# Kernel tuning notes

Measured on AMD Instinct MI355X. Metric: run time of the kernel, lower is better.

Reference implementation:

```python
import jax, jax.numpy as jnp
import numpy as np

N = 4096          # residues (2 chains x 2048)
CHAINS = 2
LMAX = 2
L = (LMAX + 1) ** 2            # 9 spherical coefficients
BBC = 32                       # bb_channels
NBB = 3                        # n_bb_atoms - 1
SPH = BBC + NBB                # 35 sphere channels fed to attention
KNN = 20
LRK = 40
HEADS = 8
HC = 32
VC = HC // 4                   # attn_value_channels = 8
EDGE_F = 32                    # 16 RBF + 16 positional
L_IDX = np.repeat(np.arange(LMAX + 1), 2 * np.arange(LMAX + 1) + 1)  # degree of each of the 9 coeffs


def so3_linear(x, w, b):
    # x: [N,L,Cin]; w: [LMAX+1,Cin,Cout] shared across m within each degree l; bias only on l=0
    out = jnp.einsum('nlc,lcd->nld', x, w[L_IDX])
    return out.at[:, 0, :].add(b)


def _rbf(d):
    mu = jnp.linspace(0.0, 20.0, 16)
    sigma = 20.0 / 16
    return jnp.exp(-(((d[..., None] - mu) / sigma) ** 2))


def _edge_pos_embed(src, dst):
    d = (src - dst).astype(jnp.float32)
    freq = jnp.exp(jnp.arange(0, 16, 2, dtype=jnp.float32) * (-np.log(10000.0) / 16))
    ang = d[:, None] * freq
    return jnp.concatenate([jnp.cos(ang), jnp.sin(ang)], axis=-1)


def setup_inputs():
    key = jax.random.key(0)
    ks = jax.random.split(key, 16)
    n = lambda i, shp, s=1.0: jax.random.normal(ks[i], shp) * s
    return {
        'X_ca': n(0, (N, 3), 10.0),
        'bb_rel': n(1, (N, NBB, 3)),
        'bb_features': n(2, (N, L, BBC)),
        'batch': jnp.repeat(jnp.arange(CHAINS), N // CHAINS),
        'x_mask': jax.random.uniform(ks[3], (N,)) < 0.02,
        'noising_mask': jax.random.uniform(ks[4], (N,)) < 0.5,
        'attn_w1': n(5, (2 * SPH + EDGE_F, HC), 0.05), 'attn_b1': jnp.zeros((HC,)),
        'attn_w2': n(6, (HC, HEADS), 0.05), 'attn_b2': jnp.zeros((HEADS,)),
        'wv': n(7, (LMAX + 1, SPH, HEADS * VC), 0.05), 'bv': jnp.zeros((HEADS * VC,)),
        'wo': n(8, (LMAX + 1, HEADS * VC, BBC), 0.05), 'bo': jnp.zeros((BBC,)),
        'wg': n(9, (BBC, BBC), 0.05), 'bg': jnp.zeros((BBC,)),
        'wf': n(10, (LMAX + 1, BBC, BBC), 0.05), 'bf': jnp.zeros((BBC,)),
        'w_xca': n(11, (LMAX + 1, BBC, 1), 0.05), 'b_xca': jnp.zeros((1,)),
        'w_gate': n(12, (BBC, 1), 0.05), 'b_gate': jnp.zeros((1,)),
        'w_bb': n(13, (LMAX + 1, BBC, NBB), 0.05), 'b_bb': jnp.zeros((NBB,)),
    }


def reference(X_ca, bb_rel, bb_features, batch, x_mask, noising_mask,
              attn_w1, attn_b1, attn_w2, attn_b2, wv, bv, wo, bo, wg, bg, wf, bf,
              w_xca, b_xca, w_gate, b_gate, w_bb, b_bb):
    Nn = X_ca.shape[0]
    BIG = jnp.float32(1e30)
    # ---- graph construction (knn_graph + sample_inv_cubic_edges) ----
    x2 = jnp.sum(X_ca * X_ca, axis=-1)
    D2 = jnp.maximum(x2[:, None] + x2[None, :] - 2.0 * (X_ca @ X_ca.T), 0.0)  # [N,N]
    same = batch[:, None] == batch[None, :]
    eye = jnp.eye(Nn, dtype=bool)
    mask_pair = x_mask[:, None] | x_mask[None, :]
    invalid = (~same) | eye | mask_pair
    knn_idx = jax.lax.top_k(-jnp.where(invalid, BIG, D2), KNN)[1]   # [N,KNN] sources per target
    # long-range: inverse-cubic distance weights, Gumbel top-k sampling, excluding knn picks
    logits = jnp.where(invalid, -BIG, -1.5 * jnp.log(D2 + 1e-6))
    rows = jnp.arange(Nn)[:, None]
    logits = logits.at[rows, knn_idx].set(-BIG)
    gumb = jax.random.gumbel(jax.random.key(1), (Nn, Nn))
    lr_idx = jax.lax.top_k(logits + gumb, LRK)[1]                   # [N,LRK]
    src = jnp.concatenate([knn_idx.reshape(-1), lr_idx.reshape(-1)])
    dst = jnp.concatenate([jnp.repeat(jnp.arange(Nn), KNN), jnp.repeat(jnp.arange(Nn), LRK)])
    # ---- edge features: RBF(dist) + relative positional embedding ----
    dvec = X_ca[src] - X_ca[dst]
    dist = jnp.linalg.norm(dvec, axis=-1)
    edge_feat = jnp.concatenate([_rbf(dist), _edge_pos_embed(src, dst)], axis=-1)  # [M,32]
    # ---- assemble SO3 node embedding [N,L,35] ----
    node = jnp.zeros((Nn, L, SPH), X_ca.dtype)
    node = node.at[:, :, :BBC].set(bb_features)
    node = node.at[:, 1:4, BBC:].set(jnp.swapaxes(bb_rel, -1, -2))  # l=1 coeffs carry bb_rel
    node = node.at[:, 0, SPH - 1].set(noising_mask.astype(X_ca.dtype))
    # ---- equivariant graph attention (simplified TransBlockV2) ----
    inv = node[:, 0, :]                                             # invariant (l=0) features
    a_in = jnp.concatenate([inv[src], inv[dst], edge_feat], axis=-1)
    h = jax.nn.silu(a_in @ attn_w1 + attn_b1)
    logit = h @ attn_w2 + attn_b2                                   # [M,HEADS]
    mx = jax.ops.segment_max(logit, dst, num_segments=Nn)
    p = jnp.exp(logit - mx[dst])
    Z = jax.ops.segment_sum(p, dst, num_segments=Nn)
    alpha = p / (Z[dst] + 1e-9)                                     # segment softmax per target/head
    v = so3_linear(node, wv, bv)[src].reshape(-1, L, HEADS, VC)     # gather source values
    msg = (v * alpha[:, None, :, None]).reshape(-1, L, HEADS * VC)
    agg = jax.ops.segment_sum(msg, dst, num_segments=Nn)            # scatter to targets
    out = so3_linear(agg, wo, bo)                                   # [N,L,32]
    gate = jax.nn.silu(out[:, 0, :] @ wg + bg)                      # invariant-gated FFN
    out = out + so3_linear(out, wf, bf) * gate[:, None, :]
    # ---- coordinate / backbone updates ----
    upd_x = so3_linear(out, w_xca, b_xca)                           # [N,L,1]
    vec = upd_x[:, 1:4, 0]                                          # l=1 -> 3-vector
    g2 = jax.nn.softplus(out[:, 0, :] @ w_gate + b_gate)            # [N,1]
    new_X = X_ca + jnp.where(noising_mask[:, None], vec * g2, 0.0)
    upd_bb = so3_linear(out, w_bb, b_bb)                            # [N,L,3]
    dbb = jnp.swapaxes(upd_bb[:, 1:4, :], -1, -2)                   # [N,3,3]
    new_bb = bb_rel + jnp.where(noising_mask[:, None, None], dbb, 0.0)
    return new_X, new_bb, out
```

## Files before the change

kernel.cpp:

```cpp
#include <hip/hip_runtime.h>
#include <hip/hip_bf16.h>
#include <stdint.h>

#define NN 4096
#define CS 2048
#define KNN 20
#define LRK 40
#define EPN 60
#define NE (NN*EPN)
#define SPHC 35
#define BBCC 32
#define NHEAD 8
#define HVD 64
#define HCD 32
#define LT 9
#define MAXC 384

#define INVAL_D2 0xFFFFFFFEu
#define CONSUMED 0xFFFFFFFFu

__device__ __forceinline__ float fast_exp(float x) {
  return __builtin_amdgcn_exp2f(x * 1.4426950408889634f);
}
__device__ __forceinline__ float fast_cos(float a) {
  float rev = a * 0.15915494309189535f;
  rev = rev - __builtin_rintf(rev);
  return __builtin_amdgcn_cosf(rev);
}
__device__ __forceinline__ float fast_sin(float a) {
  float rev = a * 0.15915494309189535f;
  rev = rev - __builtin_rintf(rev);
  return __builtin_amdgcn_sinf(rev);
}

__device__ __forceinline__ float neglogu_f(int i, int j) {
  uint32_t c = ((uint32_t)(i & 2047) << 12) | (uint32_t)j;
  const uint32_t ks0 = 0u, ks1 = 1u, ks2 = 0x1BD11BDBu;
  uint32_t x0 = c + ks0;
  uint32_t x1 = (c + 0x800000u) + ks1;
#define TF_R(r) { x0 += x1; x1 = (x1 << (r)) | (x1 >> (32 - (r))); x1 ^= x0; }
  TF_R(13) TF_R(15) TF_R(26) TF_R(6)   x0 += ks1; x1 += ks2 + 1u;
  TF_R(17) TF_R(29) TF_R(16) TF_R(24)  x0 += ks2; x1 += ks0 + 2u;
  TF_R(13) TF_R(15) TF_R(26) TF_R(6)   x0 += ks0; x1 += ks1 + 3u;
  TF_R(17) TF_R(29) TF_R(16) TF_R(24)  x0 += ks1; x1 += ks2 + 4u;
  TF_R(13) TF_R(15) TF_R(26) TF_R(6)   x0 += ks2; x1 += ks0 + 5u;
#undef TF_R
  uint32_t b = (i >= 2048) ? x1 : x0;
  float u = __uint_as_float((b >> 9) | 0x3F800000u) - 1.0f;
  u = u + 1.17549435e-38f;
  return -logf(u);
}

__global__ void prep_kernel(const float* __restrict__ X,
                            const int* __restrict__ batch,
                            const int* __restrict__ xmask,
                            float4* __restrict__ Xw, uint32_t* __restrict__ bm) {
#pragma clang fp contract(off)
  int n = blockIdx.x * blockDim.x + threadIdx.x;
  if (n >= NN) return;
  float x = X[n*3+0], y = X[n*3+1], z = X[n*3+2];
  float x2 = (x*x + y*y) + z*z;
  Xw[n] = make_float4(x, y, z, x2);
  bm[n] = ((uint32_t)batch[n] << 1) | (xmask[n] ? 1u : 0u);
}

__global__ __launch_bounds__(256) void nodeproj_kernel(const float* __restrict__ bbf,
                                                       const int* __restrict__ nmask,
                                                       const float* __restrict__ w1,
                                                       const float* __restrict__ b1,
                                                       float* __restrict__ Pn,
                                                       float* __restrict__ Pd) {
  int tid = threadIdx.x;
  int t = tid & 31;
  int n = blockIdx.x * 8 + (tid >> 5);
  float bv_ = bbf[(size_t)n * (LT*BBCC) + t];
  float an = 0.f, ad = b1[t];
  #pragma unroll 8
  for (int c = 0; c < BBCC; c++) {
    float bc = __shfl(bv_, (tid & 32) + c, 64);
    an = fmaf(bc, w1[c * HCD + t], an);
    ad = fmaf(bc, w1[(SPHC + c) * HCD + t], ad);
  }
  float nm = nmask[n] ? 1.f : 0.f;
  an = fmaf(nm, w1[34 * HCD + t], an);
  ad = fmaf(nm, w1[69 * HCD + t], ad);
  Pn[n * HCD + t] = an;
  Pd[n * HCD + t] = ad;
}

__device__ __forceinline__ void sel2l(uint32_t* val, uint32_t* hist2,
                                      uint32_t* candk, uint32_t* candp,
                                      uint32_t* sh, int* sel,
                                      int k, int base, int cb, int tid) {
  {
    uint4* h4 = (uint4*)hist2;
    uint4 z; z.x = 0; z.y = 0; z.z = 0; z.w = 0;
    h4[tid] = z; h4[tid + 256] = z;
  }
  if (tid == 0) { sh[2] = 0; sh[3] = 0; }
  __syncthreads();
  #pragma unroll
  for (int q = 0; q < 8; q++) {
    uint32_t key = val[tid + (q << 8)];
    atomicAdd(&hist2[key >> 21], 1u);
  }
  __syncthreads();
  uint32_t h[8], s = 0;
  #pragma unroll
  for (int q = 0; q < 8; q++) { h[q] = hist2[tid*8 + q]; s += h[q]; }
  uint32_t cum = s;
  #pragma unroll
  for (int off = 1; off < 64; off <<= 1) {
    uint32_t o = __shfl_up(cum, off, 64);
    if ((tid & 63) >= off) cum += o;
  }
  if ((tid & 63) == 63) sh[8 + (tid >> 6)] = cum;
  __syncthreads();
  uint32_t woff = 0;
  for (int w = 0; w < (tid >> 6); w++) woff += sh[8 + w];
  uint32_t cumAll = cum + woff;
  uint32_t cumBefore = cumAll - s;
  uint32_t rk = (uint32_t)k;
  if (rk > cumBefore && rk <= cumAll) {
    uint32_t rloc = rk - cumBefore, lp = 0;
    bool done = false;
    #pragma unroll
    for (int q = 0; q < 8; q++) {
      lp += h[q];
      if (!done && rloc <= lp) { sh[0] = (uint32_t)(tid*8 + q); sh[1] = rloc - (lp - h[q]); done = true; }
    }
  }
  __syncthreads();
  const uint32_t B = sh[0], r = sh[1];
  #pragma unroll
  for (int q = 0; q < 8; q++) {
    int pos = tid + (q << 8);
    uint32_t key = val[pos];
    if ((key >> 21) == B) {
      uint32_t idx = atomicAdd(&sh[2], 1u);
      if (idx < MAXC) { candk[idx] = key; candp[idx] = (uint32_t)pos; }
    }
  }
  __syncthreads();
  int m = (int)sh[2]; if (m > MAXC) m = MAXC;
  if (tid < 64) {
    for (int ci = tid; ci < m; ci += 64) {
      unsigned long long k64 = ((unsigned long long)candk[ci] << 32) | candp[ci];
      uint32_t rank = 0;
      for (int j = 0; j < m; j++) {
        unsigned long long o = ((unsigned long long)candk[j] << 32) | candp[j];
        rank += (o < k64) ? 1u : 0u;
      }
      if (rank == r - 1) { sh[0] = candk[ci]; sh[1] = candp[ci]; }
    }
  }
  __syncthreads();
  const uint32_t vstar = sh[0], istar = sh[1];
  #pragma unroll
  for (int q = 0; q < 8; q++) {
    int pos = tid + (q << 8);
    uint32_t key = val[pos];
    if (key < vstar || (key == vstar && (uint32_t)pos <= istar)) {
      uint32_t slot = atomicAdd(&sh[3], 1u);
      sel[base + (int)slot] = cb + pos;
    }
  }
  __syncthreads();
}

__global__ __launch_bounds__(256) void select_kernel(const float4* __restrict__ Xw,
                                                     const uint32_t* __restrict__ bm,
                                                     int* __restrict__ srcO) {
#pragma clang fp contract(off)
  __shared__ uint32_t val[CS];
  __shared__ uint32_t hist2[2048];
  __shared__ uint32_t candk[MAXC];
  __shared__ uint32_t candp[MAXC];
  __shared__ uint32_t sh[12];
  __shared__ int sel[EPN];
  const int i = blockIdx.x, tid = threadIdx.x;
  const uint32_t bmi = bm[i];

  if (bmi & 1u) {
    if (tid < KNN) srcO[(size_t)i * EPN + tid] = tid;
    else if (tid < EPN) srcO[(size_t)i * EPN + tid] = tid - KNN;
    return;
  }
  const int cb = (int)(bmi >> 1) * CS;
  const float4 xi = Xw[i];

  #pragma unroll
  for (int q = 0; q < 8; q++) {
    int pos = tid + (q << 8);
    int j = cb + pos;
    float4 xj = Xw[j];
    uint32_t bmj = bm[j];
    bool inval = ((bmj & 1u) != 0u) || (j == i);
    float dot = xi.x*xj.x + xi.y*xj.y + xi.z*xj.z;
    float d2r = (xi.w + xj.w) - 2.0f*dot;
    float d2 = d2r > 0.0f ? d2r : 0.0f;
    val[pos] = inval ? INVAL_D2 : __float_as_uint(d2);
  }
  __syncthreads();

  sel2l(val, hist2, candk, candp, sh, sel, KNN, 0, cb, tid);

  if (tid < KNN) val[sel[tid] - cb] = CONSUMED;
  __syncthreads();

  #pragma unroll
  for (int q = 0; q < 8; q++) {
    int pos = tid + (q << 8);
    uint32_t v = val[pos];
    uint32_t skey;
    if (v >= INVAL_D2) skey = CONSUMED;
    else {
      float d2p = __uint_as_float(v) + 1e-6f;
      float w = d2p * sqrtf(d2p) * neglogu_f(i, cb + pos);
      skey = __float_as_uint(w);
    }
    val[pos] = skey;
  }
  __syncthreads();

  sel2l(val, hist2, candk, candp, sh, sel, LRK, KNN, cb, tid);

  if (tid < EPN) srcO[(size_t)i * EPN + tid] = sel[tid];
}

__global__ __launch_bounds__(256) void vmat_kernel(const float* __restrict__ bbf,
                                                   const float* __restrict__ bbrel,
                                                   const int* __restrict__ nmask,
                                                   const float* __restrict__ wv,
                                                   const float* __restrict__ bv,
                                                   float* __restrict__ V) {
  int row = blockIdx.x * 4 + (threadIdx.x >> 6);
  int d = threadIdx.x & 63;
  if (row >= NN * LT) return;
  int n = row / LT, l = row % LT;
  int li = (l == 0) ? 0 : (l < 4 ? 1 : 2);
  const float* w = wv + (size_t)li * SPHC * HVD;
  float acc = (l == 0) ? bv[d] : 0.f;
  const float* nb = bbf + (size_t)(n*LT + l) * BBCC;
  for (int c = 0; c < BBCC; c++) acc = fmaf(nb[c], w[c*HVD + d], acc);
  if (l >= 1 && l < 4) {
    for (int b = 0; b < 3; b++)
      acc = fmaf(bbrel[(size_t)(n*3 + b)*3 + (l-1)], w[(32+b)*HVD + d], acc);
  }
  if (l == 0) acc = fmaf(nmask[n] ? 1.f : 0.f, w[34*HVD + d], acc);
  V[(size_t)row * HVD + d] = acc;
}

__global__ __launch_bounds__(256) void edge_kernel(const int* __restrict__ src,
                                                   const float4* __restrict__ Xw,
                                                   const float* __restrict__ Pn,
                                                   const float* __restrict__ Pd,
                                                   const float* __restrict__ w1,
                                                   const float* __restrict__ w2,
                                                   const float* __restrict__ b2,
                                                   float* __restrict__ logitO) {
  const float FR[8] = {1.0f, 0.31622776601683794f, 0.1f, 0.031622776601683794f,
                       0.01f, 0.0031622776601683794f, 0.001f, 0.00031622776601683794f};
  __shared__ float w1cf[BBCC][HCD];
  __shared__ float w2f[HCD][NHEAD];
  __shared__ float b2f[NHEAD];
  __shared__ float ef[8][BBCC];
  __shared__ float hbuf[8][HCD];
  int tid = threadIdx.x;
  for (int q = tid; q < BBCC*HCD; q += 256) w1cf[q >> 5][q & 31] = w1[70*HCD + q];
  if (tid < HCD*NHEAD) w2f[tid >> 3][tid & 7] = w2[tid];
  if (tid < NHEAD) b2f[tid] = b2[tid];
  int sub = tid >> 5, t = tid & 31;
  int e = blockIdx.x * 8 + sub;
  int d = e / EPN;
  int s = src[e];
  float4 xs = Xw[s], xd = Xw[d];
  float dx = xs.x - xd.x, dy = xs.y - xd.y, dz = xs.z - xd.z;
  float dist = sqrtf(dx*dx + dy*dy + dz*dz);
  if (t < 16) {
    float mu = (20.0f / 15.0f) * (float)t;
    float zz = (dist - mu) / 1.25f;
    ef[sub][t] = fast_exp(-zz * zz);
  } else {
    int k = t - 16;
    float del = (float)(s - d);
    float a = del * FR[k & 7];
    ef[sub][t] = (k < 8) ? fast_cos(a) : fast_sin(a);
  }
  __syncthreads();
  float a = Pn[s * HCD + t] + Pd[d * HCD + t];
  #pragma unroll
  for (int k = 0; k < BBCC; k++) a = fmaf(ef[sub][k], w1cf[k][t], a);
  hbuf[sub][t] = a / (1.f + fast_exp(-a));
  __syncthreads();
  if (tid < 64) {
    int e2 = tid >> 3, hh = tid & 7;
    float lg = b2f[hh];
    #pragma unroll
    for (int c = 0; c < HCD; c++) lg = fmaf(hbuf[e2][c], w2f[c][hh], lg);
    logitO[(size_t)(blockIdx.x * 8 + e2) * NHEAD + hh] = lg;
  }
}

__global__ __launch_bounds__(64) void node_kernel(const int* __restrict__ src,
                                                  const float* __restrict__ logit,
                                                  const float* __restrict__ V,
                                                  const float* __restrict__ wo,
                                                  const float* __restrict__ bo,
                                                  const float* __restrict__ wg,
                                                  const float* __restrict__ bg,
                                                  const float* __restrict__ wf,
                                                  const float* __restrict__ bfb,
                                                  const float* __restrict__ w_xca,
                                                  const float* __restrict__ w_gate,
                                                  const float* __restrict__ b_gate,
                                                  const float* __restrict__ w_bb,
                                                  const float* __restrict__ X,
                                                  const float* __restrict__ bbrel,
                                                  const int* __restrict__ nmask,
                                                  float* __restrict__ out) {
  const int n = blockIdx.x, t = threadIdx.x;
  __shared__ float alpha[EPN][NHEAD];
  __shared__ int slist[EPN];
  __shared__ float agg[LT][HVD];
  __shared__ float o0[LT][BBCC];
  __shared__ float ofin[LT][BBCC];
  __shared__ float gate[BBCC];
  if (t < EPN) slist[t] = src[(size_t)n * EPN + t];
  for (int q = t; q < EPN * NHEAD; q += 64) alpha[q / NHEAD][q % NHEAD] = logit[(size_t)n * 480 + q];
  __syncthreads();
  if (t < NHEAD) {
    float m = -1e30f;
    for (int e = 0; e < EPN; e++) m = fmaxf(m, alpha[e][t]);
    float Z = 0.f;
    for (int e = 0; e < EPN; e++) { float p = expf(alpha[e][t] - m); alpha[e][t] = p; Z += p; }
    float iz = 1.f / (Z + 1e-9f);
    for (int e = 0; e < EPN; e++) alpha[e][t] *= iz;
  }
  __syncthreads();
  {
    const int h = t >> 3;
    float acc[LT];
    #pragma unroll
    for (int l = 0; l < LT; l++) acc[l] = 0.f;
    for (int e = 0; e < EPN; e++) {
      const float* Vp = V + (size_t)slist[e] * (LT * HVD) + t;
      float a = alpha[e][h];
      #pragma unroll
      for (int l = 0; l < LT; l++) acc[l] = fmaf(a, Vp[l * HVD], acc[l]);
    }
    #pragma unroll
    for (int l = 0; l < LT; l++) agg[l][t] = acc[l];
  }
  __syncthreads();
  for (int idx = t; idx < LT * BBCC; idx += 64) {
    int l = idx >> 5, d = idx & 31;
    int li = (l == 0) ? 0 : (l < 4 ? 1 : 2);
    float a = (l == 0) ? bo[d] : 0.f;
    const float* w = wo + (size_t)li * HVD * BBCC;
    for (int c = 0; c < HVD; c++) a = fmaf(agg[l][c], w[c * BBCC + d], a);
    o0[l][d] = a;
  }
  __syncthreads();
  if (t < BBCC) {
    float a = bg[t];
    for (int c = 0; c < BBCC; c++) a = fmaf(o0[0][c], wg[c * BBCC + t], a);
    gate[t] = a / (1.f + expf(-a));
  }
  __syncthreads();
  for (int idx = t; idx < LT * BBCC; idx += 64) {
    int l = idx >> 5, d = idx & 31;
    int li = (l == 0) ? 0 : (l < 4 ? 1 : 2);
    float a = (l == 0) ? bfb[d] : 0.f;
    const float* w = wf + (size_t)li * BBCC * BBCC;
    for (int c = 0; c < BBCC; c++) a = fmaf(o0[l][c], w[c * BBCC + d], a);
    float r = o0[l][d] + a * gate[d];
    ofin[l][d] = r;
    out[49152 + (size_t)n * 288 + idx] = r;
  }
  __syncthreads();
  float a2 = b_gate[0];
  for (int c = 0; c < BBCC; c++) a2 = fmaf(ofin[0][c], w_gate[c], a2);
  float g2 = fmaxf(a2, 0.f) + log1pf(expf(-fabsf(a2)));
  bool noise = nmask[n] != 0;
  if (t < 3) {
    float a = 0.f;
    for (int d2 = 0; d2 < BBCC; d2++) a = fmaf(ofin[1 + t][d2], w_xca[32 + d2], a);
    float nx = X[n * 3 + t] + (noise ? a * g2 : 0.f);
    out[(size_t)n * 3 + t] = nx;
  }
  if (t < 9) {
    int b = t / 3, c = t % 3;
    float a = 0.f;
    for (int d2 = 0; d2 < BBCC; d2++) a = fmaf(ofin[1 + c][d2], w_bb[(32 + d2) * 3 + b], a);
    float nb = bbrel[(size_t)(n * 3 + b) * 3 + c] + (noise ? a : 0.f);
    out[12288 + (size_t)n * 9 + b * 3 + c] = nb;
  }
}

extern "C" void kernel_launch(void* const* d_in, const int* in_sizes, int n_in,
                              void* d_out, int out_size, void* d_ws, size_t ws_size,
                              hipStream_t stream) {
  (void)in_sizes; (void)n_in; (void)out_size;
  const float* X      = (const float*)d_in[0];
  const float* bbrel  = (const float*)d_in[1];
  const float* bbf    = (const float*)d_in[2];
  const int* batch    = (const int*)d_in[3];
  const int* xmask    = (const int*)d_in[4];
  const int* nmask    = (const int*)d_in[5];
  const float* w1     = (const float*)d_in[6];
  const float* b1     = (const float*)d_in[7];
  const float* w2     = (const float*)d_in[8];
  const float* b2     = (const float*)d_in[9];
  const float* wv     = (const float*)d_in[10];
  const float* bv     = (const float*)d_in[11];
  const float* wo     = (const float*)d_in[12];
  const float* bo     = (const float*)d_in[13];
  const float* wg     = (const float*)d_in[14];
  const float* bg     = (const float*)d_in[15];
  const float* wf     = (const float*)d_in[16];
  const float* bfb    = (const float*)d_in[17];
  const float* w_xca  = (const float*)d_in[18];
  const float* w_gate = (const float*)d_in[20];
  const float* b_gate = (const float*)d_in[21];
  const float* w_bb   = (const float*)d_in[22];

  if (ws_size < 18939904) return;
  char* ws = (char*)d_ws;
  uint32_t* bmp   = (uint32_t*)(ws + 0);
  int*      srcl  = (int*)(ws + 16384);
  float*    logit = (float*)(ws + 999424);
  float*    V     = (float*)(ws + 8863744);
  float*    Pn    = (float*)(ws + 8863744);
  float*    Pd    = (float*)(ws + 9388032);
  float4*   Xw    = (float4*)(ws + 9912320);
  float*    out   = (float*)d_out;

  prep_kernel<<<NN / 256, 256, 0, stream>>>(X, batch, xmask, Xw, bmp);
  nodeproj_kernel<<<NN / 8, 256, 0, stream>>>(bbf, nmask, w1, b1, Pn, Pd);
  select_kernel<<<NN, 256, 0, stream>>>(Xw, bmp, srcl);
  edge_kernel<<<NE / 8, 256, 0, stream>>>(srcl, Xw, Pn, Pd, w1, w2, b2, logit);
  vmat_kernel<<<(NN * LT) / 4, 256, 0, stream>>>(bbf, bbrel, nmask, wv, bv, V);
  node_kernel<<<NN, 64, 0, stream>>>(srcl, logit, V, wo, bo, wg, bg, wf, bfb,
                                     w_xca, w_gate, b_gate, w_bb, X, bbrel, nmask, out);
}
```

Before: 271.8 us.

## Merge prep, select, vmat and nodeproj into one launch; store V as bf16

Drops the separate prep, nodeproj and vmat launches and folds them, as extra block ranges, into a single graph kernel alongside the kNN/long-range selection. Positions and squared norms are now recomputed from X inline instead of read from a precomputed float4 buffer. The value matrix V is stored in bf16 and unpacked in pairs in the node kernel's aggregation loop, halving gather traffic at some precision cost. The log in the selection path also switches to the hardware log2 intrinsic. Together these aim to cut launch overhead and memory traffic, but they risk small numerical differences in neighbour selection and attention values.

New measurement: 248.4 us. -8.6%, faster.

```diff
diff --git a/kernel.cpp b/kernel.cpp
--- a/kernel.cpp
+++ b/kernel.cpp
@@ -7,7 +7,6 @@
 #define KNN 20
 #define LRK 40
 #define EPN 60
-#define NE (NN*EPN)
 #define SPHC 35
 #define BBCC 32
 #define NHEAD 8
@@ -15,9 +14,14 @@
 #define HCD 32
 #define LT 9
 #define MAXC 384
+#define VMB ((NN*LT)/4)
+#define NPB (NN/8)
 
 #define INVAL_D2 0xFFFFFFFEu
 #define CONSUMED 0xFFFFFFFFu
+
+__device__ __forceinline__ float bflo(uint32_t d) { return __uint_as_float(d << 16); }
+__device__ __forceinline__ float bfhi(uint32_t d) { return __uint_as_float(d & 0xFFFF0000u); }
 
 __device__ __forceinline__ float fast_exp(float x) {
   return __builtin_amdgcn_exp2f(x * 1.4426950408889634f);
@@ -48,44 +52,7 @@
   uint32_t b = (i >= 2048) ? x1 : x0;
   float u = __uint_as_float((b >> 9) | 0x3F800000u) - 1.0f;
   u = u + 1.17549435e-38f;
-  return -logf(u);
-}
-
-__global__ void prep_kernel(const float* __restrict__ X,
-                            const int* __restrict__ batch,
-                            const int* __restrict__ xmask,
-                            float4* __restrict__ Xw, uint32_t* __restrict__ bm) {
-#pragma clang fp contract(off)
-  int n = blockIdx.x * blockDim.x + threadIdx.x;
-  if (n >= NN) return;
-  float x = X[n*3+0], y = X[n*3+1], z = X[n*3+2];
-  float x2 = (x*x + y*y) + z*z;
-  Xw[n] = make_float4(x, y, z, x2);
-  bm[n] = ((uint32_t)batch[n] << 1) | (xmask[n] ? 1u : 0u);
-}
-
-__global__ __launch_bounds__(256) void nodeproj_kernel(const float* __restrict__ bbf,
-                                                       const int* __restrict__ nmask,
-                                                       const float* __restrict__ w1,
-                                                       const float* __restrict__ b1,
-                                                       float* __restrict__ Pn,
-                                                       float* __restrict__ Pd) {
-  int tid = threadIdx.x;
-  int t = tid & 31;
-  int n = blockIdx.x * 8 + (tid >> 5);
-  float bv_ = bbf[(size_t)n * (LT*BBCC) + t];
-  float an = 0.f, ad = b1[t];
-  #pragma unroll 8
-  for (int c = 0; c < BBCC; c++) {
-    float bc = __shfl(bv_, (tid & 32) + c, 64);
-    an = fmaf(bc, w1[c * HCD + t], an);
-    ad = fmaf(bc, w1[(SPHC + c) * HCD + t], ad);
-  }
-  float nm = nmask[n] ? 1.f : 0.f;
-  an = fmaf(nm, w1[34 * HCD + t], an);
-  ad = fmaf(nm, w1[69 * HCD + t], ad);
-  Pn[n * HCD + t] = an;
-  Pd[n * HCD + t] = ad;
+  return -0.6931471805599453f * __builtin_amdgcn_logf(u);
 }
 
 __device__ __forceinline__ void sel2l(uint32_t* val, uint32_t* hist2,
@@ -168,36 +135,83 @@
   __syncthreads();
 }
 
-__global__ __launch_bounds__(256) void select_kernel(const float4* __restrict__ Xw,
-                                                     const uint32_t* __restrict__ bm,
-                                                     int* __restrict__ srcO) {
+__global__ __launch_bounds__(256) void graph_kernel(const float* __restrict__ X,
+                                                    const int* __restrict__ batch,
+                                                    const int* __restrict__ xmask,
+                                                    const int* __restrict__ nmask,
+                                                    const float* __restrict__ bbf,
+                                                    const float* __restrict__ bbrel,
+                                                    const float* __restrict__ wv,
+                                                    const float* __restrict__ bv,
+                                                    const float* __restrict__ w1,
+                                                    const float* __restrict__ b1,
+                                                    int* __restrict__ srcO,
+                                                    __hip_bfloat16* __restrict__ V,
+                                                    float* __restrict__ Pn,
+                                                    float* __restrict__ Pd) {
 #pragma clang fp contract(off)
+  const int tid = threadIdx.x;
+  if (blockIdx.x >= NN + VMB) {
+    int t = tid & 31;
+    int n = (blockIdx.x - NN - VMB) * 8 + (tid >> 5);
+    float bv_ = bbf[(size_t)n * (LT*BBCC) + t];
+    float an = 0.f, ad = b1[t];
+    #pragma unroll 8
+    for (int c = 0; c < BBCC; c++) {
+      float bc = __shfl(bv_, (tid & 32) + c, 64);
+      an = fmaf(bc, w1[c * HCD + t], an);
+      ad = fmaf(bc, w1[(SPHC + c) * HCD + t], ad);
+    }
+    float nm = nmask[n] ? 1.f : 0.f;
+    an = fmaf(nm, w1[34 * HCD + t], an);
+    ad = fmaf(nm, w1[69 * HCD + t], ad);
+    Pn[n * HCD + t] = an;
+    Pd[n * HCD + t] = ad;
+    return;
+  }
+  if (blockIdx.x >= NN) {
+    int row = (blockIdx.x - NN) * 4 + (tid >> 6);
+    int d = tid & 63;
+    int n = row / LT, l = row % LT;
+    int li = (l == 0) ? 0 : (l < 4 ? 1 : 2);
+    const float* w = wv + (size_t)li * SPHC * HVD;
+    float acc = (l == 0) ? bv[d] : 0.f;
+    const float* nb = bbf + (size_t)(n*LT + l) * BBCC;
+    for (int c = 0; c < BBCC; c++) acc = fmaf(nb[c], w[c*HVD + d], acc);
+    if (l >= 1 && l < 4) {
+      for (int b = 0; b < 3; b++)
+        acc = fmaf(bbrel[(size_t)(n*3 + b)*3 + (l-1)], w[(32+b)*HVD + d], acc);
+    }
+    if (l == 0) acc = fmaf(nmask[n] ? 1.f : 0.f, w[34*HVD + d], acc);
+    V[(size_t)row * HVD + d] = __float2bfloat16(acc);
+    return;
+  }
   __shared__ uint32_t val[CS];
   __shared__ uint32_t hist2[2048];
   __shared__ uint32_t candk[MAXC];
   __shared__ uint32_t candp[MAXC];
   __shared__ uint32_t sh[12];
   __shared__ int sel[EPN];
-  const int i = blockIdx.x, tid = threadIdx.x;
-  const uint32_t bmi = bm[i];
-
-  if (bmi & 1u) {
+  const int i = blockIdx.x;
+
+  if (xmask[i]) {
     if (tid < KNN) srcO[(size_t)i * EPN + tid] = tid;
     else if (tid < EPN) srcO[(size_t)i * EPN + tid] = tid - KNN;
     return;
   }
-  const int cb = (int)(bmi >> 1) * CS;
-  const float4 xi = Xw[i];
+  const int cb = batch[i] * CS;
+  const float xi0 = X[i*3+0], xi1 = X[i*3+1], xi2 = X[i*3+2];
+  const float x2i = (xi0*xi0 + xi1*xi1) + xi2*xi2;
 
   #pragma unroll
   for (int q = 0; q < 8; q++) {
     int pos = tid + (q << 8);
     int j = cb + pos;
-    float4 xj = Xw[j];
-    uint32_t bmj = bm[j];
-    bool inval = ((bmj & 1u) != 0u) || (j == i);
-    float dot = xi.x*xj.x + xi.y*xj.y + xi.z*xj.z;
-    float d2r = (xi.w + xj.w) - 2.0f*dot;
+    float xj0 = X[j*3+0], xj1 = X[j*3+1], xj2 = X[j*3+2];
+    float x2j = (xj0*xj0 + xj1*xj1) + xj2*xj2;
+    bool inval = (xmask[j] != 0) || (j == i);
+    float dot = xi0*xj0 + xi1*xj1 + xi2*xj2;
+    float d2r = (x2i + x2j) - 2.0f*dot;
     float d2 = d2r > 0.0f ? d2r : 0.0f;
     val[pos] = inval ? INVAL_D2 : __float_as_uint(d2);
   }
@@ -228,31 +242,8 @@
   if (tid < EPN) srcO[(size_t)i * EPN + tid] = sel[tid];
 }
 
-__global__ __launch_bounds__(256) void vmat_kernel(const float* __restrict__ bbf,
-                                                   const float* __restrict__ bbrel,
-                                                   const int* __restrict__ nmask,
-                                                   const float* __restrict__ wv,
-                                                   const float* __restrict__ bv,
-                                                   float* __restrict__ V) {
-  int row = blockIdx.x * 4 + (threadIdx.x >> 6);
-  int d = threadIdx.x & 63;
-  if (row >= NN * LT) return;
-  int n = row / LT, l = row % LT;
-  int li = (l == 0) ? 0 : (l < 4 ? 1 : 2);
-  const float* w = wv + (size_t)li * SPHC * HVD;
-  float acc = (l == 0) ? bv[d] : 0.f;
-  const float* nb = bbf + (size_t)(n*LT + l) * BBCC;
-  for (int c = 0; c < BBCC; c++) acc = fmaf(nb[c], w[c*HVD + d], acc);
-  if (l >= 1 && l < 4) {
-    for (int b = 0; b < 3; b++)
-      acc = fmaf(bbrel[(size_t)(n*3 + b)*3 + (l-1)], w[(32+b)*HVD + d], acc);
-  }
-  if (l == 0) acc = fmaf(nmask[n] ? 1.f : 0.f, w[34*HVD + d], acc);
-  V[(size_t)row * HVD + d] = acc;
-}
-
 __global__ __launch_bounds__(256) void edge_kernel(const int* __restrict__ src,
-                                                   const float4* __restrict__ Xw,
+                                                   const float* __restrict__ X,
                                                    const float* __restrict__ Pn,
                                                    const float* __restrict__ Pd,
                                                    const float* __restrict__ w1,
@@ -274,8 +265,9 @@
   int e = blockIdx.x * 8 + sub;
   int d = e / EPN;
   int s = src[e];
-  float4 xs = Xw[s], xd = Xw[d];
-  float dx = xs.x - xd.x, dy = xs.y - xd.y, dz = xs.z - xd.z;
+  float dx = X[s*3+0] - X[d*3+0];
+  float dy = X[s*3+1] - X[d*3+1];
+  float dz = X[s*3+2] - X[d*3+2];
   float dist = sqrtf(dx*dx + dy*dy + dz*dz);
   if (t < 16) {
     float mu = (20.0f / 15.0f) * (float)t;
@@ -304,7 +296,7 @@
 
 __global__ __launch_bounds__(64) void node_kernel(const int* __restrict__ src,
                                                   const float* __restrict__ logit,
-                                                  const float* __restrict__ V,
+                                                  const __hip_bfloat16* __restrict__ V,
                                                   const float* __restrict__ wo,
                                                   const float* __restrict__ bo,
                                                   const float* __restrict__ wg,
@@ -327,7 +319,7 @@
   __shared__ float ofin[LT][BBCC];
   __shared__ float gate[BBCC];
   if (t < EPN) slist[t] = src[(size_t)n * EPN + t];
-  for (int q = t; q < EPN * NHEAD; q += 64) alpha[q / NHEAD][q % NHEAD] = logit[(size_t)n * 480 + q];
+  for (int q = t; q < EPN * NHEAD; q += 64) alpha[q >> 3][q & 7] = logit[(size_t)n * 480 + q];
   __syncthreads();
   if (t < NHEAD) {
     float m = -1e30f;
@@ -339,18 +331,30 @@
   }
   __syncthreads();
   {
-    const int h = t >> 3;
-    float acc[LT];
-    #pragma unroll
-    for (int l = 0; l < LT; l++) acc[l] = 0.f;
+    const int h = (t & 31) >> 2;
+    const bool tail = (t < 32);
+    float a0 = 0.f, a1 = 0.f, a2 = 0.f, a3 = 0.f, a4 = 0.f;
+    float b0 = 0.f, b1_ = 0.f, b2_ = 0.f, b3 = 0.f, b4 = 0.f;
     for (int e = 0; e < EPN; e++) {
-      const float* Vp = V + (size_t)slist[e] * (LT * HVD) + t;
+      const uint32_t* Vr = (const uint32_t*)(V + (size_t)slist[e] * (LT * HVD));
+      uint32_t d0 = Vr[t];
+      uint32_t d1 = Vr[t + 64];
+      uint32_t d2 = Vr[t + 128];
+      uint32_t d3 = Vr[t + 192];
+      uint32_t d4 = tail ? Vr[t + 256] : 0u;
       float a = alpha[e][h];
-      #pragma unroll
-      for (int l = 0; l < LT; l++) acc[l] = fmaf(a, Vp[l * HVD], acc[l]);
-    }
-    #pragma unroll
-    for (int l = 0; l < LT; l++) agg[l][t] = acc[l];
+      a0 = fmaf(a, bflo(d0), a0);  b0  = fmaf(a, bfhi(d0), b0);
+      a1 = fmaf(a, bflo(d1), a1);  b1_ = fmaf(a, bfhi(d1), b1_);
+      a2 = fmaf(a, bflo(d2), a2);  b2_ = fmaf(a, bfhi(d2), b2_);
+      a3 = fmaf(a, bflo(d3), a3);  b3  = fmaf(a, bfhi(d3), b3);
+      a4 = fmaf(a, bflo(d4), a4);  b4  = fmaf(a, bfhi(d4), b4);
+    }
+    const int l0 = t >> 5, c = 2 * (t & 31);
+    agg[l0 + 0][c] = a0;  agg[l0 + 0][c + 1] = b0;
+    agg[l0 + 2][c] = a1;  agg[l0 + 2][c + 1] = b1_;
+    agg[l0 + 4][c] = a2;  agg[l0 + 4][c + 1] = b2_;
+    agg[l0 + 6][c] = a3;  agg[l0 + 6][c + 1] = b3;
+    if (tail) { agg[8][c] = a4;  agg[8][c + 1] = b4; }
   }
   __syncthreads();
   for (int idx = t; idx < LT * BBCC; idx += 64) {
@@ -379,22 +383,24 @@
     out[49152 + (size_t)n * 288 + idx] = r;
   }
   __syncthreads();
-  float a2 = b_gate[0];
-  for (int c = 0; c < BBCC; c++) a2 = fmaf(ofin[0][c], w_gate[c], a2);
-  float g2 = fmaxf(a2, 0.f) + log1pf(expf(-fabsf(a2)));
-  bool noise = nmask[n] != 0;
-  if (t < 3) {
-    float a = 0.f;
-    for (int d2 = 0; d2 < BBCC; d2++) a = fmaf(ofin[1 + t][d2], w_xca[32 + d2], a);
-    float nx = X[n * 3 + t] + (noise ? a * g2 : 0.f);
-    out[(size_t)n * 3 + t] = nx;
-  }
-  if (t < 9) {
-    int b = t / 3, c = t % 3;
-    float a = 0.f;
-    for (int d2 = 0; d2 < BBCC; d2++) a = fmaf(ofin[1 + c][d2], w_bb[(32 + d2) * 3 + b], a);
-    float nb = bbrel[(size_t)(n * 3 + b) * 3 + c] + (noise ? a : 0.f);
-    out[12288 + (size_t)n * 9 + b * 3 + c] = nb;
+  if (t < 16) {
+    float a2 = b_gate[0];
+    for (int c = 0; c < BBCC; c++) a2 = fmaf(ofin[0][c], w_gate[c], a2);
+    float g2 = fmaxf(a2, 0.f) + log1pf(expf(-fabsf(a2)));
+    bool noise = nmask[n] != 0;
+    if (t < 3) {
+      float a = 0.f;
+      for (int d2 = 0; d2 < BBCC; d2++) a = fmaf(ofin[1 + t][d2], w_xca[32 + d2], a);
+      float nx = X[n * 3 + t] + (noise ? a * g2 : 0.f);
+      out[(size_t)n * 3 + t] = nx;
+    }
+    if (t < 9) {
+      int b = t / 3, c = t % 3;
+      float a = 0.f;
+      for (int d2 = 0; d2 < BBCC; d2++) a = fmaf(ofin[1 + c][d2], w_bb[(32 + d2) * 3 + b], a);
+      float nb = bbrel[(size_t)(n * 3 + b) * 3 + c] + (noise ? a : 0.f);
+      out[12288 + (size_t)n * 9 + b * 3 + c] = nb;
+    }
   }
 }
 
@@ -427,20 +433,16 @@
 
   if (ws_size < 18939904) return;
   char* ws = (char*)d_ws;
-  uint32_t* bmp   = (uint32_t*)(ws + 0);
-  int*      srcl  = (int*)(ws + 16384);
-  float*    logit = (float*)(ws + 999424);
-  float*    V     = (float*)(ws + 8863744);
-  float*    Pn    = (float*)(ws + 8863744);
-  float*    Pd    = (float*)(ws + 9388032);
-  float4*   Xw    = (float4*)(ws + 9912320);
+  int*      srcl  = (int*)(ws + 0);
+  float*    logit = (float*)(ws + 983040);
+  __hip_bfloat16* V = (__hip_bfloat16*)(ws + 8847360);
+  float*    Pn    = (float*)(ws + 13565952);
+  float*    Pd    = (float*)(ws + 14090240);
   float*    out   = (float*)d_out;
 
-  prep_kernel<<<NN / 256, 256, 0, stream>>>(X, batch, xmask, Xw, bmp);
-  nodeproj_kernel<<<NN / 8, 256, 0, stream>>>(bbf, nmask, w1, b1, Pn, Pd);
-  select_kernel<<<NN, 256, 0, stream>>>(Xw, bmp, srcl);
-  edge_kernel<<<NE / 8, 256, 0, stream>>>(srcl, Xw, Pn, Pd, w1, w2, b2, logit);
-  vmat_kernel<<<(NN * LT) / 4, 256, 0, stream>>>(bbf, bbrel, nmask, wv, bv, V);
+  graph_kernel<<<NN + VMB + NPB, 256, 0, stream>>>(X, batch, xmask, nmask, bbf, bbrel,
+                                                   wv, bv, w1, b1, srcl, V, Pn, Pd);
+  edge_kernel<<<(NN * EPN) / 8, 256, 0, stream>>>(srcl, X, Pn, Pd, w1, w2, b2, logit);
   node_kernel<<<NN, 64, 0, stream>>>(srcl, logit, V, wo, bo, wg, bg, wf, bfb,
                                      w_xca, w_gate, b_gate, w_bb, X, bbrel, nmask, out);
 }
```
